# Optimization experiments

Measured on AMD Instinct MI355X. Metric: run time of the kernel, lower is better.

## Reference

```python
import jax, jax.numpy as jnp
import numpy as np


def setup_inputs() -> dict:
    key = jax.random.key(0)
    k1, k2 = jax.random.split(key)
    B, T, I, H, D = 32, 2048, 512, 16, 64
    x = jax.random.normal(k1, (B, T, I), dtype=jnp.float32)
    # glorot-ish scale keeps q.k scores in a stable range for exp()
    kvq_kernel = jax.random.normal(k2, (I, H, D, 3), dtype=jnp.float32) * 0.02
    return {"x": x, "kvq_kernel": kvq_kernel}


def reference(x, kvq_kernel):
    # x: (B, T, I); kvq_kernel: (I, H, D, 3)
    B, T, I = x.shape
    _, H, D, _ = kvq_kernel.shape
    # Per-timestep projection (same einsum '...i,ihok->...hok' as the cell, batched over T)
    kvq = jnp.einsum('bti,ihok->bthok', x, kvq_kernel)  # (B,T,H,D,3)
    # tf.split order: k, v, q
    k = kvq[..., 0]
    v = kvq[..., 1]
    q = kvq[..., 2]
    # time-major stack for scan: (T, 3, B, H, D)
    qkv = jnp.stack([q, k, v], axis=0).transpose(2, 0, 1, 3, 4)

    num0 = jnp.zeros((B, H, D), dtype=x.dtype)
    den0 = jnp.zeros((B, H), dtype=x.dtype)
    max0 = jnp.zeros((B, H), dtype=x.dtype)  # keras zero initial state

    def step(carry, qkv_t):
        num, den, mx = carry
        qt, kt, vt = qkv_t[0], qkv_t[1], qkv_t[2]  # each (B,H,D)
        s = jnp.einsum('bhd,bhd->bh', qt, kt)       # per-head score
        cmax = jnp.maximum(mx, s)                   # running max (online softmax)
        md = jnp.exp(mx - cmax)                     # rescale factor for old stats
        sm = jnp.exp(s - cmax)
        den_n = den * md + sm
        num_n = num * md[..., None] + vt * sm[..., None]
        h = num_n / den_n[..., None]                # (B,H,D)
        o = h.sum(axis=-2)                          # concat_heads=False -> sum over heads
        return (num_n, den_n, cmax), o

    _, outs = jax.lax.scan(step, (num0, den0, max0), qkv)  # (T,B,D)
    return outs.transpose(1, 0, 2)  # (B,T,D)
```

## Files before the change

### kernel.cpp

```cpp
#include <hip/hip_runtime.h>
#include <stdint.h>

#define B_   32
#define T_   2048
#define I_   512
#define H_   16
#define D_   64
#define BT   (B_*T_)
#define CCH  64
#define LCH  (T_/CCH)


typedef short short8 __attribute__((ext_vector_type(8)));
typedef float floatx4 __attribute__((ext_vector_type(4)));

__device__ __forceinline__ unsigned short f2bf(float f) {
    uint32_t u = __float_as_uint(f);
    u = (u + 0x7FFFu + ((u >> 16) & 1u)) >> 16;
    return (unsigned short)u;
}
__device__ __forceinline__ float bf2f(unsigned short u) {
    return __uint_as_float(((uint32_t)u) << 16);
}

__global__ __launch_bounds__(256) void k_convert_x(const float* __restrict__ x,
                                                   unsigned short* __restrict__ xb) {
    int i = blockIdx.x * 256 + threadIdx.x;
    float4 v = ((const float4*)x)[i];
    ushort4 o;
    o.x = f2bf(v.x); o.y = f2bf(v.y); o.z = f2bf(v.z); o.w = f2bf(v.w);
    ((ushort4*)xb)[i] = o;
}

__global__ __launch_bounds__(256) void k_repack_w(const float* __restrict__ W,
                                                  unsigned short* __restrict__ Wt) {
    int idx = blockIdx.x * 256 + threadIdx.x;
    if (idx >= I_ * H_ * D_ * 3) return;
    int kk = idx % 3;
    int d  = (idx / 3) % D_;
    int h  = (idx / (3 * D_)) % H_;
    int i  = idx / (3 * D_ * H_);
    int col = (kk == 1) ? (2048 + h * 64 + d)
                        : (h * 128 + d + (kk == 2 ? 64 : 0));
    Wt[(size_t)col * I_ + i] = f2bf(W[idx]);
}

__device__ __forceinline__ void load_lds16(const void* g, void* l) {
    __builtin_amdgcn_global_load_lds((const __attribute__((address_space(1))) unsigned int*)g,
                                     (__attribute__((address_space(3))) unsigned int*)l, 16, 0, 0);
}

__global__ __launch_bounds__(256) void k_gemm(const unsigned short* __restrict__ A,
                                              const unsigned short* __restrict__ Bt,
                                              unsigned short* __restrict__ Vb,
                                              float* __restrict__ s_arr) {
    __shared__ unsigned short Alds[128 * 32];
    __shared__ unsigned short Blds[128 * 32];
    const int tid  = threadIdx.x;
    const int lane = tid & 63;
    const int wave = tid >> 6;
    const int cb = blockIdx.x;
    const int rb = blockIdx.y;
    const int l15 = lane & 15;
    const int kh  = lane >> 4;

    if (cb < 16) {
        floatx4 acc[2][8] = {};
        for (int ko = 0; ko < 16; ++ko) {
            const int k0 = ko * 32;
            #pragma unroll
            for (int it = 0; it < 2; ++it) {
                int lin = it * 256 + wave * 64 + lane;
                int r = lin >> 2;
                int c = (lin & 3) << 3;
                load_lds16(A  + (size_t)(rb * 128 + r) * I_ + k0 + c,
                           (void*)(Alds + (size_t)(it * 256 + wave * 64) * 8));
                load_lds16(Bt + (size_t)(cb * 128 + r) * I_ + k0 + c,
                           (void*)(Blds + (size_t)(it * 256 + wave * 64) * 8));
            }
            __syncthreads();
            short8 af[2], bfr[8];
            #pragma unroll
            for (int m = 0; m < 2; ++m)
                af[m] = *(const short8*)(Alds + (size_t)(wave * 32 + m * 16 + l15) * 32 + kh * 8);
            #pragma unroll
            for (int n = 0; n < 8; ++n)
                bfr[n] = *(const short8*)(Blds + (size_t)(n * 16 + l15) * 32 + kh * 8);
            #pragma unroll
            for (int m = 0; m < 2; ++m)
                #pragma unroll
                for (int n = 0; n < 8; ++n)
                    acc[m][n] = __builtin_amdgcn_mfma_f32_16x16x32_bf16(af[m], bfr[n], acc[m][n], 0, 0, 0);
            __syncthreads();
        }
        float sacc[2][4];
        #pragma unroll
        for (int m = 0; m < 2; ++m)
            #pragma unroll
            for (int reg = 0; reg < 4; ++reg) {
                float s = 0.f;
                #pragma unroll
                for (int n = 0; n < 4; ++n)
                    s += acc[m][n][reg] * acc[m][n + 4][reg];
                sacc[m][reg] = s;
            }
        #pragma unroll
        for (int m = 0; m < 2; ++m)
            #pragma unroll
            for (int reg = 0; reg < 4; ++reg) {
                float s = sacc[m][reg];
                s += __shfl_xor(s, 1);
                s += __shfl_xor(s, 2);
                s += __shfl_xor(s, 4);
                s += __shfl_xor(s, 8);
                sacc[m][reg] = s;
            }
        float sv = sacc[0][0];
        #pragma unroll
        for (int m = 0; m < 2; ++m)
            #pragma unroll
            for (int reg = 0; reg < 4; ++reg)
                if (l15 == m * 4 + reg) sv = sacc[m][reg];
        if (l15 < 8) {
            int row = rb * 128 + wave * 32 + (l15 >> 2) * 16 + kh * 4 + (l15 & 3);
            int b = row >> 11, t = row & 2047;
            s_arr[((size_t)(b * H_ + cb) << 11) + t] = sv;
        }
    } else {
        const int wr = wave >> 1, wc = wave & 1;
        floatx4 acc[4][4] = {};
        for (int ko = 0; ko < 16; ++ko) {
            const int k0 = ko * 32;
            #pragma unroll
            for (int it = 0; it < 2; ++it) {
                int lin = it * 256 + wave * 64 + lane;
                int r = lin >> 2;
                int c = (lin & 3) << 3;
                load_lds16(A  + (size_t)(rb * 128 + r) * I_ + k0 + c,
                           (void*)(Alds + (size_t)(it * 256 + wave * 64) * 8));
                load_lds16(Bt + (size_t)(cb * 128 + r) * I_ + k0 + c,
                           (void*)(Blds + (size_t)(it * 256 + wave * 64) * 8));
            }
            __syncthreads();
            short8 af[4], bfr[4];
            #pragma unroll
            for (int m = 0; m < 4; ++m)
                af[m] = *(const short8*)(Alds + (size_t)(wr * 64 + m * 16 + l15) * 32 + kh * 8);
            #pragma unroll
            for (int n = 0; n < 4; ++n)
                bfr[n] = *(const short8*)(Blds + (size_t)(wc * 64 + n * 16 + l15) * 32 + kh * 8);
            #pragma unroll
            for (int m = 0; m < 4; ++m)
                #pragma unroll
                for (int n = 0; n < 4; ++n)
                    acc[m][n] = __builtin_amdgcn_mfma_f32_16x16x32_bf16(af[m], bfr[n], acc[m][n], 0, 0, 0);
            __syncthreads();
        }
        #pragma unroll
        for (int m = 0; m < 4; ++m) {
            #pragma unroll
            for (int n = 0; n < 4; ++n) {
                int vcol = (cb - 16) * 128 + wc * 64 + n * 16 + l15;
                size_t rrow = (size_t)rb * 128 + wr * 64 + m * 16 + kh * 4;
                #pragma unroll
                for (int reg = 0; reg < 4; ++reg)
                    Vb[(rrow + reg) * 1024 + vcol] = f2bf(acc[m][n][reg]);
            }
        }
    }
}

__global__ __launch_bounds__(256) void k_sumchunk(const unsigned short* __restrict__ Vb,
                                                  const float* __restrict__ s_arr,
                                                  float* __restrict__ m_arr,
                                                  float* __restrict__ d_arr,
                                                  float* __restrict__ n_arr) {
    const int wave = threadIdx.x >> 6, lane = threadIdx.x & 63;
    const int chunk = blockIdx.x * 4 + wave;
    const int c  = chunk & (CCH - 1);
    const int bh = chunk >> 6;
    const int h  = bh & (H_ - 1);
    const int b  = bh >> 4;

    float sval = (lane < 32) ? s_arr[(size_t)bh * T_ + c * LCH + lane] : -INFINITY;
    float M = sval;
    #pragma unroll
    for (int off = 32; off; off >>= 1) M = fmaxf(M, __shfl_xor(M, off));
    float wt_l = (lane < 32) ? __expf(sval - M) : 0.f;
    float Dh = wt_l;
    #pragma unroll
    for (int off = 32; off; off >>= 1) Dh += __shfl_xor(Dh, off);

    float Nh = 0.f;
    size_t base_v = ((size_t)b * T_ + c * LCH) * 1024 + h * D_ + lane;
    #pragma unroll
    for (int t = 0; t < LCH; ++t) {
        float vd = bf2f(Vb[base_v + (size_t)t * 1024]);
        Nh += __shfl(wt_l, t) * vd;
    }
    if (lane == 0) { m_arr[chunk] = M; d_arr[chunk] = Dh; }
    n_arr[(size_t)chunk * 64 + lane] = Nh;
}

__global__ __launch_bounds__(256) void k_prefix2(const float* __restrict__ m_arr,
                                                 const float* __restrict__ d_arr,
                                                 const float* __restrict__ n_arr,
                                                 float* __restrict__ Zb,
                                                 float* __restrict__ pdb,
                                                 float* __restrict__ pnb) {
    const int wave = threadIdx.x >> 6, lane = threadIdx.x & 63;
    const int bh = blockIdx.x * 4 + wave;
    float m = -INFINITY, den = 0.f, n = 0.f;
    for (int c = 0; c < CCH; ++c) {
        int idx = bh * CCH + c;
        float mc = m_arr[idx], dc = d_arr[idx];
        float nc = n_arr[(size_t)idx * 64 + lane];
        float Z = fmaxf(m, mc);
        float beta = __expf(m - Z);
        if (lane == 0) { Zb[idx] = Z; pdb[idx] = den * beta; }
        pnb[(size_t)idx * 64 + lane] = n * beta;
        float a2 = __expf(mc - Z);
        den = den * beta + dc * a2;
        n   = n * beta + nc * a2;
        m = Z;
    }
}

__global__ __launch_bounds__(256) void k_final(const unsigned short* __restrict__ Vb,
                                               const float* __restrict__ s_arr,
                                               const float* __restrict__ Zb,
                                               const float* __restrict__ pdb,
                                               const float* __restrict__ pnb,
                                               float* __restrict__ out) {
    __shared__ float red[4][LCH * 64];
    const int tid = threadIdx.x;
    const int wave = tid >> 6, lane = tid & 63;
    const int bc = blockIdx.x;
    const int c = bc & (CCH - 1), b = bc >> 6;

    float csum[LCH];
    #pragma unroll
    for (int t = 0; t < LCH; ++t) csum[t] = 0.f;

    #pragma unroll
    for (int hh = 0; hh < 4; ++hh) {
        const int h = wave * 4 + hh;
        const int bh = b * H_ + h;
        const int chain = bh * CCH + c;
        const float Z  = Zb[chain];
        const float pd = pdb[chain];
        const float pnbv = pnb[(size_t)chain * 64 + lane];

        float sval = (lane < 32) ? s_arr[(size_t)bh * T_ + c * LCH + lane] : 0.f;
        float wv = (lane < 32) ? __expf(sval - Z) : 0.f;
        float cum = wv;
        #pragma unroll
        for (int off = 1; off < 32; off <<= 1) {
            float o = __shfl_up(cum, off, 32);
            if ((lane & 31) >= off) cum += o;
        }
        float rv = __builtin_amdgcn_rcpf(pd + cum);

        float num = 0.f;
        size_t vbase = ((size_t)b * T_ + c * LCH) * 1024 + h * D_ + lane;
        #pragma unroll
        for (int t = 0; t < LCH; ++t) {
            float vd = bf2f(Vb[vbase + (size_t)t * 1024]);
            float wt = __shfl(wv, t);
            float rt = __shfl(rv, t);
            num += wt * vd;
            csum[t] += (pnbv + num) * rt;
        }
    }

    #pragma unroll
    for (int t = 0; t < LCH; ++t)
        red[wave][t * 64 + lane] = csum[t];
    __syncthreads();

    size_t ob = ((size_t)b * T_ + c * LCH) * 64;
    #pragma unroll
    for (int i = 0; i < 8; ++i) {
        int idx = i * 256 + tid;
        out[ob + idx] = red[0][idx] + red[1][idx] + red[2][idx] + red[3][idx];
    }
}

extern "C" void kernel_launch(void* const* d_in, const int* in_sizes, int n_in,
                              void* d_out, int out_size, void* d_ws, size_t ws_size,
                              hipStream_t stream) {
    const float* x = (const float*)d_in[0];
    const float* W = (const float*)d_in[1];
    float* out = (float*)d_out;
    char* ws = (char*)d_ws;

    unsigned short* Vb  = (unsigned short*)(ws);
    unsigned short* xb  = (unsigned short*)(ws + 134217728ull);
    unsigned short* Wt  = (unsigned short*)(ws + 201326592ull);
    float* s_arr = (float*)(ws + 204472320ull);
    float* m_arr = (float*)(ws + 208666624ull);
    float* d_arr = (float*)(ws + 208797696ull);
    float* n_arr = (float*)(ws + 208928768ull);
    float* Zb    = (float*)(ws + 217317376ull);
    float* pdb   = (float*)(ws + 217448448ull);
    float* pnb   = (float*)(ws + 217579520ull);

    k_convert_x<<<(BT * I_ / 4) / 256, 256, 0, stream>>>(x, xb);
    k_repack_w<<<(I_ * H_ * D_ * 3 + 255) / 256, 256, 0, stream>>>(W, Wt);
    k_gemm<<<dim3(24, BT / 128), 256, 0, stream>>>(xb, Wt, Vb, s_arr);
    k_sumchunk<<<(B_ * H_ * CCH) / 4, 256, 0, stream>>>(Vb, s_arr, m_arr, d_arr, n_arr);
    k_prefix2<<<(B_ * H_) / 4, 256, 0, stream>>>(m_arr, d_arr, n_arr, Zb, pdb, pnb);
    k_final<<<B_ * CCH, 256, 0, stream>>>(Vb, s_arr, Zb, pdb, pnb, out);
}
```

Before: 546.7 us.

## Store V head-major and pre-swizzle LDS tiles for fragment-contiguous MFMA reads

The projection kernel now stages A/B tiles in LDS in MFMA-fragment order, so each lane's short8 read is contiguous. V is written in a (b,h,t,d) layout instead of row-major 1024-wide rows. With that layout the chunk-sum and final kernels can load 16-byte vectors of eight d values per lane and do the in-chunk prefix over time with cross-lane shuffle scans. This replaces the strided 2-byte gathers with coalesced vector loads, at the cost of more shuffles and scattered 2-byte stores in the GEMM epilogue.

New measurement: 691.6 us. 26.5% more time.

```diff
diff --git a/kernel.cpp b/kernel.cpp
--- a/kernel.cpp
+++ b/kernel.cpp
@@ -70,22 +70,24 @@
             const int k0 = ko * 32;
             #pragma unroll
             for (int it = 0; it < 2; ++it) {
-                int lin = it * 256 + wave * 64 + lane;
-                int r = lin >> 2;
-                int c = (lin & 3) << 3;
-                load_lds16(A  + (size_t)(rb * 128 + r) * I_ + k0 + c,
+                int c = it * 256 + tid;
+                int fragidx = c >> 4;
+                int l15c = c & 15;
+                int rowgrp = fragidx >> 2;
+                int ks = fragidx & 3;
+                load_lds16(A  + (size_t)(rb * 128 + rowgrp * 16 + l15c) * I_ + k0 + ks * 8,
                            (void*)(Alds + (size_t)(it * 256 + wave * 64) * 8));
-                load_lds16(Bt + (size_t)(cb * 128 + r) * I_ + k0 + c,
+                load_lds16(Bt + (size_t)(cb * 128 + rowgrp * 16 + l15c) * I_ + k0 + ks * 8,
                            (void*)(Blds + (size_t)(it * 256 + wave * 64) * 8));
             }
             __syncthreads();
             short8 af[2], bfr[8];
             #pragma unroll
             for (int m = 0; m < 2; ++m)
-                af[m] = *(const short8*)(Alds + (size_t)(wave * 32 + m * 16 + l15) * 32 + kh * 8);
+                af[m] = *(const short8*)(Alds + (size_t)(wave * 2 + m) * 512 + kh * 128 + l15 * 8);
             #pragma unroll
             for (int n = 0; n < 8; ++n)
-                bfr[n] = *(const short8*)(Blds + (size_t)(n * 16 + l15) * 32 + kh * 8);
+                bfr[n] = *(const short8*)(Blds + (size_t)n * 512 + kh * 128 + l15 * 8);
             #pragma unroll
             for (int m = 0; m < 2; ++m)
                 #pragma unroll
@@ -133,22 +135,24 @@
             const int k0 = ko * 32;
             #pragma unroll
             for (int it = 0; it < 2; ++it) {
-                int lin = it * 256 + wave * 64 + lane;
-                int r = lin >> 2;
-                int c = (lin & 3) << 3;
-                load_lds16(A  + (size_t)(rb * 128 + r) * I_ + k0 + c,
+                int c = it * 256 + tid;
+                int fragidx = c >> 4;
+                int l15c = c & 15;
+                int rowgrp = fragidx >> 2;
+                int ks = fragidx & 3;
+                load_lds16(A  + (size_t)(rb * 128 + rowgrp * 16 + l15c) * I_ + k0 + ks * 8,
                            (void*)(Alds + (size_t)(it * 256 + wave * 64) * 8));
-                load_lds16(Bt + (size_t)(cb * 128 + r) * I_ + k0 + c,
+                load_lds16(Bt + (size_t)(cb * 128 + rowgrp * 16 + l15c) * I_ + k0 + ks * 8,
                            (void*)(Blds + (size_t)(it * 256 + wave * 64) * 8));
             }
             __syncthreads();
             short8 af[4], bfr[4];
             #pragma unroll
             for (int m = 0; m < 4; ++m)
-                af[m] = *(const short8*)(Alds + (size_t)(wr * 64 + m * 16 + l15) * 32 + kh * 8);
+                af[m] = *(const short8*)(Alds + (size_t)(wr * 4 + m) * 512 + kh * 128 + l15 * 8);
             #pragma unroll
             for (int n = 0; n < 4; ++n)
-                bfr[n] = *(const short8*)(Blds + (size_t)(wc * 64 + n * 16 + l15) * 32 + kh * 8);
+                bfr[n] = *(const short8*)(Blds + (size_t)(wc * 4 + n) * 512 + kh * 128 + l15 * 8);
             #pragma unroll
             for (int m = 0; m < 4; ++m)
                 #pragma unroll
@@ -156,15 +160,18 @@
                     acc[m][n] = __builtin_amdgcn_mfma_f32_16x16x32_bf16(af[m], bfr[n], acc[m][n], 0, 0, 0);
             __syncthreads();
         }
+        const int b_idx = rb >> 4;
+        const int h = (cb - 16) * 2 + wc;
+        const int t0 = (rb & 15) * 128 + wr * 64 + kh * 4;
         #pragma unroll
         for (int m = 0; m < 4; ++m) {
             #pragma unroll
             for (int n = 0; n < 4; ++n) {
-                int vcol = (cb - 16) * 128 + wc * 64 + n * 16 + l15;
-                size_t rrow = (size_t)rb * 128 + wr * 64 + m * 16 + kh * 4;
+                int d = n * 16 + l15;
+                size_t base = ((size_t)(b_idx * H_ + h) * T_ + t0 + m * 16) * 64 + d;
                 #pragma unroll
                 for (int reg = 0; reg < 4; ++reg)
-                    Vb[(rrow + reg) * 1024 + vcol] = f2bf(acc[m][n][reg]);
+                    Vb[base + (size_t)reg * 64] = f2bf(acc[m][n][reg]);
             }
         }
     }
@@ -179,8 +186,7 @@
     const int chunk = blockIdx.x * 4 + wave;
     const int c  = chunk & (CCH - 1);
     const int bh = chunk >> 6;
-    const int h  = bh & (H_ - 1);
-    const int b  = bh >> 4;
+    const int tg = lane >> 3, g8 = lane & 7;
 
     float sval = (lane < 32) ? s_arr[(size_t)bh * T_ + c * LCH + lane] : -INFINITY;
     float M = sval;
@@ -191,15 +197,27 @@
     #pragma unroll
     for (int off = 32; off; off >>= 1) Dh += __shfl_xor(Dh, off);
 
-    float Nh = 0.f;
-    size_t base_v = ((size_t)b * T_ + c * LCH) * 1024 + h * D_ + lane;
-    #pragma unroll
-    for (int t = 0; t < LCH; ++t) {
-        float vd = bf2f(Vb[base_v + (size_t)t * 1024]);
-        Nh += __shfl(wt_l, t) * vd;
-    }
+    float Nh[8] = {};
+    size_t vbase = ((size_t)bh * T_ + c * LCH) * 64;
+    #pragma unroll
+    for (int i = 0; i < 4; ++i) {
+        short8 v8 = *(const short8*)(Vb + vbase + (size_t)(i * 64 + lane) * 8);
+        float w = __shfl(wt_l, i * 8 + tg);
+        #pragma unroll
+        for (int j = 0; j < 8; ++j) Nh[j] += w * bf2f((unsigned short)v8[j]);
+    }
+    #pragma unroll
+    for (int off = 8; off < 64; off <<= 1)
+        #pragma unroll
+        for (int j = 0; j < 8; ++j) Nh[j] += __shfl_xor(Nh[j], off);
+
     if (lane == 0) { m_arr[chunk] = M; d_arr[chunk] = Dh; }
-    n_arr[(size_t)chunk * 64 + lane] = Nh;
+    if (lane < 8) {
+        float4 a = {Nh[0], Nh[1], Nh[2], Nh[3]};
+        float4 bq = {Nh[4], Nh[5], Nh[6], Nh[7]};
+        *(float4*)(n_arr + (size_t)chunk * 64 + lane * 8)     = a;
+        *(float4*)(n_arr + (size_t)chunk * 64 + lane * 8 + 4) = bq;
+    }
 }
 
 __global__ __launch_bounds__(256) void k_prefix2(const float* __restrict__ m_arr,
@@ -235,12 +253,11 @@
     __shared__ float red[4][LCH * 64];
     const int tid = threadIdx.x;
     const int wave = tid >> 6, lane = tid & 63;
+    const int tg = lane >> 3, g8 = lane & 7;
     const int bc = blockIdx.x;
     const int c = bc & (CCH - 1), b = bc >> 6;
 
-    float csum[LCH];
-    #pragma unroll
-    for (int t = 0; t < LCH; ++t) csum[t] = 0.f;
+    float acc[4][8] = {};
 
     #pragma unroll
     for (int hh = 0; hh < 4; ++hh) {
@@ -249,7 +266,9 @@
         const int chain = bh * CCH + c;
         const float Z  = Zb[chain];
         const float pd = pdb[chain];
-        const float pnbv = pnb[(size_t)chain * 64 + lane];
+        float4 p0 = *(const float4*)(pnb + (size_t)chain * 64 + g8 * 8);
+        float4 p1 = *(const float4*)(pnb + (size_t)chain * 64 + g8 * 8 + 4);
+        float pn8[8] = {p0.x, p0.y, p0.z, p0.w, p1.x, p1.y, p1.z, p1.w};
 
         float sval = (lane < 32) ? s_arr[(size_t)bh * T_ + c * LCH + lane] : 0.f;
         float wv = (lane < 32) ? __expf(sval - Z) : 0.f;
@@ -261,21 +280,40 @@
         }
         float rv = __builtin_amdgcn_rcpf(pd + cum);
 
-        float num = 0.f;
-        size_t vbase = ((size_t)b * T_ + c * LCH) * 1024 + h * D_ + lane;
-        #pragma unroll
-        for (int t = 0; t < LCH; ++t) {
-            float vd = bf2f(Vb[vbase + (size_t)t * 1024]);
-            float wt = __shfl(wv, t);
-            float rt = __shfl(rv, t);
-            num += wt * vd;
-            csum[t] += (pnbv + num) * rt;
-        }
-    }
-
-    #pragma unroll
-    for (int t = 0; t < LCH; ++t)
-        red[wave][t * 64 + lane] = csum[t];
+        float carry[8] = {};
+        size_t vbase = ((size_t)bh * T_ + c * LCH) * 64;
+        #pragma unroll
+        for (int i = 0; i < 4; ++i) {
+            short8 v8 = *(const short8*)(Vb + vbase + (size_t)(i * 64 + lane) * 8);
+            float w = __shfl(wv, i * 8 + tg);
+            float r = __shfl(rv, i * 8 + tg);
+            float val[8];
+            #pragma unroll
+            for (int j = 0; j < 8; ++j) val[j] = w * bf2f((unsigned short)v8[j]);
+            #pragma unroll
+            for (int off = 8; off < 64; off <<= 1) {
+                #pragma unroll
+                for (int j = 0; j < 8; ++j) {
+                    float o = __shfl_up(val[j], off);
+                    if (lane >= off) val[j] += o;
+                }
+            }
+            #pragma unroll
+            for (int j = 0; j < 8; ++j)
+                acc[i][j] += (pn8[j] + carry[j] + val[j]) * r;
+            #pragma unroll
+            for (int j = 0; j < 8; ++j)
+                carry[j] += __shfl(val[j], 56 + g8);
+        }
+    }
+
+    #pragma unroll
+    for (int i = 0; i < 4; ++i) {
+        float4 a = {acc[i][0], acc[i][1], acc[i][2], acc[i][3]};
+        float4 bq = {acc[i][4], acc[i][5], acc[i][6], acc[i][7]};
+        *(float4*)(&red[wave][(i * 8 + tg) * 64 + g8 * 8])     = a;
+        *(float4*)(&red[wave][(i * 8 + tg) * 64 + g8 * 8 + 4]) = bq;
+    }
     __syncthreads();
 
     size_t ob = ((size_t)b * T_ + c * LCH) * 64;
```
